# Kernel tuning notes

Measured on AMD Instinct MI355X. Metric: run time of the kernel, lower is better.

Reference implementation:

```python
import jax, jax.numpy as jnp
import numpy as np

VOXEL_SIZE = np.array([0.05, 0.05, 0.1], np.float32)
PC_RANGE = np.array([0.0, -40.0, -3.0, 70.4, 40.0, 1.0], np.float32)
GRID = np.round((PC_RANGE[3:] - PC_RANGE[:3]) / VOXEL_SIZE).astype(np.int64)  # [1408, 1600, 40]
MAX_POINTS = 35
MAX_VOXELS = 120000
N_POINTS = 1_500_000


def setup_inputs() -> dict:
    key = jax.random.key(0)
    k1, k2 = jax.random.split(key)
    u = jax.random.uniform(k1, (N_POINTS, 3), dtype=jnp.float32)
    lo = jnp.array([-2.0, -42.0, -3.5], jnp.float32)   # slightly outside range -> some points dropped
    hi = jnp.array([72.0, 42.0, 1.5], jnp.float32)
    xyz = lo + u * (hi - lo)
    feat = jax.random.uniform(k2, (N_POINTS, 1), dtype=jnp.float32)
    return {"points": jnp.concatenate([xyz, feat], axis=1)}


def _voxelize(points):
    """Deterministic hard voxelization (mmcv hard_voxelize_forward semantics).

    Returns fixed-shape (jit-friendly) padded outputs plus voxel_num; the
    original CUDA op returns the first voxel_num rows of each array.
    """
    N = points.shape[0]
    gx, gy, gz = int(GRID[0]), int(GRID[1]), int(GRID[2])
    n_cells = gx * gy * gz
    vsz = jnp.asarray(VOXEL_SIZE)
    lo = jnp.asarray(PC_RANGE[:3])

    c = jnp.floor((points[:, :3] - lo) / vsz).astype(jnp.int64)          # [N,3] voxel coord (x,y,z)
    valid = jnp.all((c >= 0) & (c < jnp.array([gx, gy, gz])), axis=1)    # remove_outside_points=True
    lin = c[:, 2] * (gy * gx) + c[:, 1] * gx + c[:, 0]                    # linear voxel id
    key_ = jnp.where(valid, lin, n_cells)                                 # sentinel bin for invalid

    pos = jnp.arange(N, dtype=jnp.int64)
    order = jnp.argsort(key_ * N + pos)                # stable sort by voxel key (composite key)
    skey = key_[order]
    is_start = jnp.concatenate([jnp.ones((1,), bool), skey[1:] != skey[:-1]])
    gid = jnp.cumsum(is_start) - 1                      # group id per sorted position

    g_start = jax.ops.segment_min(pos, gid, num_segments=N)
    slot = pos - g_start[gid]                           # arrival-order slot within voxel
    rep = jax.ops.segment_min(order, gid, num_segments=N)   # first original index per group
    g_key = jax.ops.segment_min(skey, gid, num_segments=N)
    g_valid = g_key < n_cells

    # voxel ids assigned in order of first point occurrence (deterministic variant)
    rep_s = jnp.where(g_valid, rep, N)
    rank = jnp.zeros(N, jnp.int64).at[jnp.argsort(rep_s)].set(pos)   # inverse permutation = rank
    vox_of_group = jnp.where(g_valid & (rank < MAX_VOXELS), rank, -1)

    v = vox_of_group[gid]                               # voxel id per sorted point (-1 dropped)
    keep = (v >= 0) & (slot < MAX_POINTS)
    vid = jnp.where(v >= 0, v, MAX_VOXELS)              # OOB index -> dropped by mode='drop'

    voxels = jnp.zeros((MAX_VOXELS, MAX_POINTS, points.shape[1]), points.dtype)
    voxels = voxels.at[vid, slot].set(points[order], mode='drop')

    npts = jax.ops.segment_sum(keep.astype(jnp.int32), jnp.where(keep, v, MAX_VOXELS),
                               num_segments=MAX_VOXELS + 1)[:MAX_VOXELS]

    czyx = c[:, ::-1].astype(jnp.int32)                 # mmcv stores coors as (z, y, x)
    g_idx = jnp.where(vox_of_group >= 0, vox_of_group, MAX_VOXELS)
    coors = jnp.zeros((MAX_VOXELS, 3), jnp.int32).at[g_idx].set(
        czyx[jnp.clip(rep, 0, N - 1)], mode='drop')

    voxel_num = jnp.minimum(jnp.sum(g_valid.astype(jnp.int32)), MAX_VOXELS)
    return voxels, coors, npts, voxel_num


def reference(points):
    return _voxelize(points)
```

## Files before the change

### kernel.cpp

```cpp
#include <hip/hip_runtime.h>
#include <stdint.h>
#include <stdio.h>


#define GXc 1408
#define GYc 1600
#define GXY (GXc * GYc)
#define MAXV 120000
#define MAXP 35
#define MPREFIX 180224
#define TBITS 20
#define TSIZE (1u << TBITS)
#define TMASK (TSIZE - 1u)
#define EMPTY64 0xFFFFFFFFFFFFFFFFull
#define INV32 0xFFFFFFFFu
#define SCAN_B 256
#define SCAN_I 8
#define SCAN_TILE (SCAN_B * SCAN_I)
#define OUT_ELEMS ((size_t)MAXV * MAXP * 4 + (size_t)MAXV * 3 + (size_t)MAXV + 1)

typedef unsigned long long u64;

__global__ void Voxelization_50345606644201_kernel() {}

__device__ __forceinline__ uint32_t mix32(uint32_t x) {
    x ^= x >> 16; x *= 0x85ebca6bu;
    x ^= x >> 13; x *= 0xc2b2ae35u;
    x ^= x >> 16;
    return x;
}

__device__ __forceinline__ float bfr(float f) {
    union { float f; uint32_t u; } v; v.f = f;
    v.u = (v.u + 0x7FFFu + ((v.u >> 16) & 1u)) & 0xFFFF0000u;
    return v.f;
}

struct Cell { int cx, cy, cz; int valid; };

__device__ __forceinline__ Cell cell_of(float4 p) {
    float fx = floorf((p.x - 0.0f)     / 0.05f);
    float fy = floorf((p.y - (-40.0f)) / 0.05f);
    float fz = floorf((p.z - (-3.0f))  / 0.1f);
    Cell c;
    c.valid = (fx >= 0.0f) && (fx < 1408.0f) &&
              (fy >= 0.0f) && (fy < 1600.0f) &&
              (fz >= 0.0f) && (fz < 40.0f);
    c.cx = (int)fx; c.cy = (int)fy; c.cz = (int)fz;
    return c;
}

__global__ void k_init(u64* __restrict__ table, uint32_t* __restrict__ sig32,
                       uint32_t* __restrict__ flags32,
                       uint32_t* __restrict__ dupeflag32, uint32_t nfw,
                       uint32_t* __restrict__ misc) {
    uint32_t stride = gridDim.x * blockDim.x;
    uint32_t tid = blockIdx.x * blockDim.x + threadIdx.x;
    for (uint32_t j = tid; j < TSIZE; j += stride) table[j] = EMPTY64;
    for (uint32_t j = tid; j < TSIZE / 4u; j += stride) sig32[j] = 0u;
    for (uint32_t j = tid; j < nfw; j += stride) { flags32[j] = 0u; dupeflag32[j] = 0u; }
    if (tid == 0) { misc[0] = 0u; misc[1] = 0u; }
}

__global__ void k_pointsA(const float4* __restrict__ pts, int M,
                          u64* __restrict__ table, uint8_t* __restrict__ sig,
                          uint8_t* __restrict__ dupeflag,
                          uint32_t* __restrict__ gclaims) {
    __shared__ uint32_t scl;
    if (threadIdx.x == 0) scl = 0u;
    __syncthreads();
    uint32_t claims = 0;
    int base = blockIdx.x * (blockDim.x * 4) + threadIdx.x;
    #pragma unroll
    for (int r = 0; r < 4; r++) {
        int i = base + r * blockDim.x;
        if (i < M) {
            float4 p = pts[i];
            Cell c = cell_of(p);
            if (c.valid) {
                uint32_t lin = (uint32_t)c.cz * (uint32_t)GXY
                             + (uint32_t)c.cy * (uint32_t)GXc + (uint32_t)c.cx;
                uint32_t full = mix32(lin);
                uint32_t h = full & TMASK;
                uint8_t mysig = (uint8_t)((full >> 24) | 1u);
                u64 val = ((u64)(uint32_t)i << 32) | (u64)lin;
                for (uint32_t probes = 0; probes <= TMASK; probes++) {
                    u64 prev = atomicCAS(&table[h], EMPTY64, val);
                    if (prev == EMPTY64) {
                        sig[h] = mysig;
                        claims++;
                        break;
                    }
                    if ((uint32_t)prev == lin) {
                        u64 old = atomicMin(&table[h], val);
                        uint32_t loser = (val < old) ? (uint32_t)(old >> 32)
                                                     : (uint32_t)i;
                        dupeflag[loser] = 1u;
                        break;
                    }
                    h = (h + 1u) & TMASK;
                }
            }
        }
    }
    if (claims) atomicAdd(&scl, claims);
    __syncthreads();
    if (threadIdx.x == 0 && scl) atomicAdd(gclaims, scl);
}

__global__ void k_pointsB(const float4* __restrict__ pts, int M, int n,
                          u64* __restrict__ table, uint8_t* __restrict__ sig,
                          uint8_t* __restrict__ dupeflag,
                          const uint32_t* __restrict__ gclaims) {
    int i = M + blockIdx.x * blockDim.x + threadIdx.x;
    if (i >= n) return;
    float4 p = pts[i];
    Cell c = cell_of(p);
    if (!c.valid) return;
    uint32_t lin = (uint32_t)c.cz * (uint32_t)GXY
                 + (uint32_t)c.cy * (uint32_t)GXc + (uint32_t)c.cx;
    uint32_t full = mix32(lin);
    uint32_t h = full & TMASK;
    uint8_t mysig = (uint8_t)((full >> 24) | 1u);
    if (*gclaims >= (uint32_t)MAXV) {
        for (uint32_t probes = 0; probes <= TMASK; probes++) {
            uint8_t s = sig[h];
            if (s == 0u) return;
            if (s == mysig) {
                u64 e = table[h];
                if ((uint32_t)e == lin) { dupeflag[i] = 1u; return; }
            }
            h = (h + 1u) & TMASK;
        }
        return;
    }
    u64 val = ((u64)(uint32_t)i << 32) | (u64)lin;
    for (uint32_t probes = 0; probes <= TMASK; probes++) {
        u64 e = table[h];
        if ((uint32_t)e == lin) { dupeflag[i] = 1u; return; }
        if (e == EMPTY64) {
            u64 prev = atomicCAS(&table[h], EMPTY64, val);
            if (prev == EMPTY64) { sig[h] = mysig; return; }
            if ((uint32_t)prev == lin) {
                u64 old = atomicMin(&table[h], val);
                uint32_t loser = (val < old) ? (uint32_t)(old >> 32) : (uint32_t)i;
                dupeflag[loser] = 1u;
                return;
            }
        }
        h = (h + 1u) & TMASK;
    }
}

__global__ void k_sweep(const u64* __restrict__ table,
                        uint8_t* __restrict__ flags) {
    uint32_t stride = gridDim.x * blockDim.x;
    uint32_t tid = blockIdx.x * blockDim.x + threadIdx.x;
    for (uint32_t j = tid; j < TSIZE; j += stride) {
        u64 e = table[j];
        if (e != EMPTY64) flags[(uint32_t)(e >> 32)] = 1u;
    }
}

__device__ __forceinline__ uint32_t flag_at(const uint8_t* __restrict__ flags,
                                            int i, int n) {
    return (i < n) ? (uint32_t)flags[i] : 0u;
}

__global__ void k_scanA(const uint8_t* __restrict__ flags, int n,
                        uint32_t* __restrict__ bsums) {
    __shared__ uint32_t sh[SCAN_B];
    int t = threadIdx.x;
    int myStart = blockIdx.x * SCAN_TILE + t * SCAN_I;
    uint32_t s = 0;
    #pragma unroll
    for (int j = 0; j < SCAN_I; j++) s += flag_at(flags, myStart + j, n);
    sh[t] = s; __syncthreads();
    for (int off = SCAN_B / 2; off > 0; off >>= 1) {
        if (t < off) sh[t] += sh[t + off];
        __syncthreads();
    }
    if (t == 0) bsums[blockIdx.x] = sh[0];
}

__global__ void k_scanC(const float4* __restrict__ pts,
                        const uint8_t* __restrict__ flags, int n, int nb,
                        const uint32_t* __restrict__ bsums,
                        uint32_t* __restrict__ vrank,
                        float* __restrict__ coors,
                        uint32_t* __restrict__ cnt,
                        uint32_t* __restrict__ slotsrc,
                        float4* __restrict__ vox4,
                        uint32_t* __restrict__ tot,
                        float* __restrict__ voxnum) {
    __shared__ uint32_t sh[SCAN_B];
    __shared__ uint32_t exoff_sh;
    int t = threadIdx.x;
    int bid = blockIdx.x;
    uint32_t part = 0;
    for (int j = t; j < bid; j += SCAN_B) part += bsums[j];
    sh[t] = part; __syncthreads();
    for (int off = SCAN_B / 2; off > 0; off >>= 1) {
        if (t < off) sh[t] += sh[t + off];
        __syncthreads();
    }
    if (t == 0) exoff_sh = sh[0];
    __syncthreads();
    uint32_t exoff = exoff_sh;
    __syncthreads();
    int myStart = bid * SCAN_TILE + t * SCAN_I;
    uint32_t f[SCAN_I];
    uint32_t lsum = 0;
    #pragma unroll
    for (int j = 0; j < SCAN_I; j++) {
        f[j] = flag_at(flags, myStart + j, n);
        lsum += f[j];
    }
    sh[t] = lsum; __syncthreads();
    for (int off = 1; off < SCAN_B; off <<= 1) {
        uint32_t add = (t >= off) ? sh[t - off] : 0u;
        __syncthreads();
        sh[t] += add;
        __syncthreads();
    }
    if (bid == nb - 1 && t == 0) {
        uint32_t total = exoff + sh[SCAN_B - 1];
        *tot = total;
        uint32_t vn = total < (uint32_t)MAXV ? total : (uint32_t)MAXV;
        *voxnum = bfr((float)vn);
    }
    uint32_t rank = exoff + (sh[t] - lsum);
    for (int j = 0; j < SCAN_I; j++) {
        if (f[j]) {
            int i = myStart + j;
            if (rank < (uint32_t)MAXV) {
                vrank[i] = rank;
                float4 p = pts[i];
                Cell c = cell_of(p);
                size_t cb = (size_t)rank * 3;
                coors[cb + 0] = bfr((float)c.cz);
                coors[cb + 1] = bfr((float)c.cy);
                coors[cb + 2] = bfr((float)c.cx);
                uint32_t base = rank * (uint32_t)MAXP;
                cnt[rank] = 1u;
                slotsrc[base] = (uint32_t)i;
                vox4[base] = make_float4(bfr(p.x), bfr(p.y), bfr(p.z), bfr(p.w));
            } else {
                vrank[i] = INV32;
            }
            rank++;
        }
    }
}

__global__ void k_dupes(const float4* __restrict__ pts,
                        const u64* __restrict__ table,
                        const uint32_t* __restrict__ vrank,
                        const uint8_t* __restrict__ dupeflag, int n,
                        uint32_t* __restrict__ cnt,
                        uint32_t* __restrict__ slotsrc,
                        float4* __restrict__ vox4) {
    int stride = gridDim.x * blockDim.x;
    for (int i = blockIdx.x * blockDim.x + threadIdx.x; i < n; i += stride) {
        if (!dupeflag[i]) continue;
        float4 p = pts[i];
        Cell c = cell_of(p);
        uint32_t lin = (uint32_t)c.cz * (uint32_t)GXY
                     + (uint32_t)c.cy * (uint32_t)GXc + (uint32_t)c.cx;
        uint32_t h = mix32(lin) & TMASK;
        uint32_t mi = INV32;
        for (uint32_t probes = 0; probes <= TMASK; probes++) {
            u64 e = table[h];
            if ((uint32_t)e == lin) { mi = (uint32_t)(e >> 32); break; }
            if (e == EMPTY64) break;
            h = (h + 1u) & TMASK;
        }
        if (mi == INV32) continue;
        uint32_t v = vrank[mi];
        if (v >= (uint32_t)MAXV) continue;
        uint32_t s = atomicAdd(&cnt[v], 1u);
        if (s < (uint32_t)MAXP) {
            uint32_t idx = v * (uint32_t)MAXP + s;
            slotsrc[idx] = (uint32_t)i;
            vox4[idx] = make_float4(bfr(p.x), bfr(p.y), bfr(p.z), bfr(p.w));
        }
    }
}

__global__ void k_final(const uint32_t* __restrict__ cnt,
                        uint32_t* __restrict__ slotsrc,
                        float4* __restrict__ vox4,
                        float* __restrict__ npts,
                        const uint32_t* __restrict__ tot) {
    int v = blockIdx.x * blockDim.x + threadIdx.x;
    if (v >= MAXV) return;
    uint32_t total = *tot;
    if ((uint32_t)v >= total) { npts[v] = 0.0f; return; }
    uint32_t c = cnt[v];
    uint32_t m = c < (uint32_t)MAXP ? c : (uint32_t)MAXP;
    npts[v] = bfr((float)m);
    if (m >= 2u) {
        uint32_t base = (uint32_t)v * (uint32_t)MAXP;
        for (uint32_t a = 0; a + 1u < m; a++) {
            uint32_t best = a, bi = slotsrc[base + a];
            for (uint32_t b = a + 1u; b < m; b++) {
                uint32_t ti = slotsrc[base + b];
                if (ti < bi) { bi = ti; best = b; }
            }
            if (best != a) {
                uint32_t ta = slotsrc[base + a];
                slotsrc[base + a] = slotsrc[base + best];
                slotsrc[base + best] = ta;
                float4 va = vox4[base + a];
                vox4[base + a] = vox4[base + best];
                vox4[base + best] = va;
            }
        }
    }
}

extern "C" void kernel_launch(void* const* d_in, const int* in_sizes, int n_in,
                              void* d_out, int out_size, void* d_ws, size_t ws_size,
                              hipStream_t stream) {
    (void)n_in; (void)out_size;
    const float4* pts = (const float4*)d_in[0];
    int n = in_sizes[0] / 4;
    int M = MPREFIX < n ? MPREFIX : n;

    float* out    = (float*)d_out;
    float* coors  = out + (size_t)MAXV * MAXP * 4;
    float* npts   = coors + (size_t)MAXV * 3;
    float* voxnum = out + (OUT_ELEMS - 1);

    size_t npad = ((size_t)n + 255) & ~(size_t)255;
    size_t off = 0;
    size_t oT = off;  off += (size_t)TSIZE * 8;
    size_t oSg = off; off += (size_t)TSIZE;
    size_t oF = off;  off += npad;
    size_t oDF = off; off += npad;
    size_t oV = off;  off += (size_t)n * 4;
    off = (off + 255) & ~(size_t)255;
    size_t oC = off;  off += (size_t)MAXV * 4;
    off = (off + 255) & ~(size_t)255;
    size_t oB = off;  off += 4096;
    size_t oX = off;  off += 256;
    size_t oS = off;  off += (size_t)MAXV * MAXP * 4;
    size_t need = off;

    if (need > ws_size) return;

    char* w = (char*)d_ws;
    u64*      table    = (u64*)(w + oT);
    uint8_t*  sig      = (uint8_t*)(w + oSg);
    uint8_t*  flags    = (uint8_t*)(w + oF);
    uint8_t*  dupeflag = (uint8_t*)(w + oDF);
    uint32_t* vrank    = (uint32_t*)(w + oV);
    uint32_t* cnt      = (uint32_t*)(w + oC);
    uint32_t* bsums    = (uint32_t*)(w + oB);
    uint32_t* misc     = (uint32_t*)(w + oX);
    uint32_t* tot      = misc;
    uint32_t* gclaims  = misc + 1;
    uint32_t* slotsrc  = (uint32_t*)(w + oS);

    int nbA    = (M + 1023) / 1024;
    int nbB    = (n - M + 255) / 256;
    int nbScan = (n + SCAN_TILE - 1) / SCAN_TILE;
    uint32_t nfw = ((uint32_t)npad) / 4u;

    k_init<<<2048, 256, 0, stream>>>(table, (uint32_t*)sig, (uint32_t*)flags,
                                     (uint32_t*)dupeflag, nfw, misc);
    k_pointsA<<<nbA, 256, 0, stream>>>(pts, M, table, sig, dupeflag, gclaims);
    if (n > M)
        k_pointsB<<<nbB, 256, 0, stream>>>(pts, M, n, table, sig, dupeflag,
                                           gclaims);
    k_sweep<<<2048, 256, 0, stream>>>(table, flags);
    k_scanA<<<nbScan, SCAN_B, 0, stream>>>(flags, n, bsums);
    k_scanC<<<nbScan, SCAN_B, 0, stream>>>(pts, flags, n, nbScan, bsums,
                                           vrank, coors, cnt, slotsrc,
                                           (float4*)out, tot, voxnum);
    k_dupes<<<1024, 256, 0, stream>>>(pts, table, vrank, dupeflag, n,
                                      cnt, slotsrc, (float4*)out);
    k_final<<<(MAXV + 255) / 256, 256, 0, stream>>>(cnt, slotsrc, (float4*)out,
                                                    npts, tot);

    hipStreamCaptureStatus cs = hipStreamCaptureStatusNone;
    (void)hipStreamIsCapturing(stream, &cs);
    if (cs == hipStreamCaptureStatusNone) {
        static uint32_t h_tot, h_cl; static float h_vn;
        h_tot = 0; h_cl = 0; h_vn = -1.0f;
        (void)hipStreamSynchronize(stream);
        (void)hipMemcpyAsync(&h_tot, tot, 4, hipMemcpyDeviceToHost, stream);
        (void)hipMemcpyAsync(&h_cl, gclaims, 4, hipMemcpyDeviceToHost, stream);
        (void)hipMemcpyAsync(&h_vn, voxnum, 4, hipMemcpyDeviceToHost, stream);
        (void)hipStreamSynchronize(stream);
        fprintf(stderr, "[vox r21] n=%d M=%d claims=%u tot=%u voxnum=%.1f\n",
                n, M, h_cl, h_tot, h_vn);
        fflush(stderr);
    }
}
```

Before: 61.50 us.

## Drop block-sum scan kernel; compute prefix by popcount and skip frozen blocks

Removes the separate block-sum kernel. Each scan block now computes its exclusive offset directly by popcounting the flag bytes before its tile, which assumes each flag byte is 0 or 1. When the global claim count already reaches the voxel cap, blocks past the prefix region exit early and the totals are written from the claim counter. This saves a launch and most of the scan work in the saturated case. The cost is a redundant O(n) prefix read per block, which grows quadratically across blocks.

```diff
diff --git a/kernel.cpp b/kernel.cpp
--- a/kernel.cpp
+++ b/kernel.cpp
@@ -167,25 +167,9 @@
     return (i < n) ? (uint32_t)flags[i] : 0u;
 }
 
-__global__ void k_scanA(const uint8_t* __restrict__ flags, int n,
-                        uint32_t* __restrict__ bsums) {
-    __shared__ uint32_t sh[SCAN_B];
-    int t = threadIdx.x;
-    int myStart = blockIdx.x * SCAN_TILE + t * SCAN_I;
-    uint32_t s = 0;
-    #pragma unroll
-    for (int j = 0; j < SCAN_I; j++) s += flag_at(flags, myStart + j, n);
-    sh[t] = s; __syncthreads();
-    for (int off = SCAN_B / 2; off > 0; off >>= 1) {
-        if (t < off) sh[t] += sh[t + off];
-        __syncthreads();
-    }
-    if (t == 0) bsums[blockIdx.x] = sh[0];
-}
-
 __global__ void k_scanC(const float4* __restrict__ pts,
-                        const uint8_t* __restrict__ flags, int n, int nb,
-                        const uint32_t* __restrict__ bsums,
+                        const uint8_t* __restrict__ flags, int n, int nb, int M,
+                        const uint32_t* __restrict__ gclaims,
                         uint32_t* __restrict__ vrank,
                         float* __restrict__ coors,
                         uint32_t* __restrict__ cnt,
@@ -197,8 +181,19 @@
     __shared__ uint32_t exoff_sh;
     int t = threadIdx.x;
     int bid = blockIdx.x;
+    int start = bid * SCAN_TILE;
+    bool frozen = (*gclaims >= (uint32_t)MAXV);
+    if (frozen) {
+        if (bid == 0 && t == 0) {
+            *tot = *gclaims;
+            *voxnum = bfr((float)MAXV);
+        }
+        if (start >= M) return;
+    }
+    const uint32_t* f32 = (const uint32_t*)flags;
+    int nwords = start >> 2;
     uint32_t part = 0;
-    for (int j = t; j < bid; j += SCAN_B) part += bsums[j];
+    for (int j = t; j < nwords; j += SCAN_B) part += (uint32_t)__popc(f32[j]);
     sh[t] = part; __syncthreads();
     for (int off = SCAN_B / 2; off > 0; off >>= 1) {
         if (t < off) sh[t] += sh[t + off];
@@ -208,7 +203,7 @@
     __syncthreads();
     uint32_t exoff = exoff_sh;
     __syncthreads();
-    int myStart = bid * SCAN_TILE + t * SCAN_I;
+    int myStart = start + t * SCAN_I;
     uint32_t f[SCAN_I];
     uint32_t lsum = 0;
     #pragma unroll
@@ -223,7 +218,7 @@
         sh[t] += add;
         __syncthreads();
     }
-    if (bid == nb - 1 && t == 0) {
+    if (!frozen && bid == nb - 1 && t == 0) {
         uint32_t total = exoff + sh[SCAN_B - 1];
         *tot = total;
         uint32_t vn = total < (uint32_t)MAXV ? total : (uint32_t)MAXV;
@@ -342,7 +337,6 @@
     off = (off + 255) & ~(size_t)255;
     size_t oC = off;  off += (size_t)MAXV * 4;
     off = (off + 255) & ~(size_t)255;
-    size_t oB = off;  off += 4096;
     size_t oX = off;  off += 256;
     size_t oS = off;  off += (size_t)MAXV * MAXP * 4;
     size_t need = off;
@@ -356,7 +350,6 @@
     uint8_t*  dupeflag = (uint8_t*)(w + oDF);
     uint32_t* vrank    = (uint32_t*)(w + oV);
     uint32_t* cnt      = (uint32_t*)(w + oC);
-    uint32_t* bsums    = (uint32_t*)(w + oB);
     uint32_t* misc     = (uint32_t*)(w + oX);
     uint32_t* tot      = misc;
     uint32_t* gclaims  = misc + 1;
@@ -374,8 +367,7 @@
         k_pointsB<<<nbB, 256, 0, stream>>>(pts, M, n, table, sig, dupeflag,
                                            gclaims);
     k_sweep<<<2048, 256, 0, stream>>>(table, flags);
-    k_scanA<<<nbScan, SCAN_B, 0, stream>>>(flags, n, bsums);
-    k_scanC<<<nbScan, SCAN_B, 0, stream>>>(pts, flags, n, nbScan, bsums,
+    k_scanC<<<nbScan, SCAN_B, 0, stream>>>(pts, flags, n, nbScan, M, gclaims,
                                            vrank, coors, cnt, slotsrc,
                                            (float4*)out, tot, voxnum);
     k_dupes<<<1024, 256, 0, stream>>>(pts, table, vrank, dupeflag, n,
@@ -393,7 +385,7 @@
         (void)hipMemcpyAsync(&h_cl, gclaims, 4, hipMemcpyDeviceToHost, stream);
         (void)hipMemcpyAsync(&h_vn, voxnum, 4, hipMemcpyDeviceToHost, stream);
         (void)hipStreamSynchronize(stream);
-        fprintf(stderr, "[vox r21] n=%d M=%d claims=%u tot=%u voxnum=%.1f\n",
+        fprintf(stderr, "[vox r22] n=%d M=%d claims=%u tot=%u voxnum=%.1f\n",
                 n, M, h_cl, h_tot, h_vn);
         fflush(stderr);
     }
```

Result: slower. 78.07 us (+27.0%).
